# Kernel tuning notes

Hardware: AMD Instinct MI355X
Metric: run time of the kernel (lower is better)

The kernel has to match this reference:

```python
import jax, jax.numpy as jnp
import numpy as np

DIM = 64
NUM_HEAD = 4
C_IN = 2 * DIM                      # dim * proj_ratio
N_PER_HEAD = C_IN // NUM_HEAD       # 32
M_TRI = N_PER_HEAD * (N_PER_HEAD + 1) // 2   # 528
C_POOL = NUM_HEAD * M_TRI           # 2112 == dim*(dim+2)/2
EPS = 1e-5


def setup_inputs() -> dict:
    key = jax.random.key(0)
    ks = jax.random.split(key, 8)
    B, H, W = 4, 128, 128
    x = jax.random.normal(ks[0], (B, C_IN, H, W), dtype=jnp.float32)
    norm1_w = 1.0 + 0.1 * jax.random.normal(ks[1], (C_IN,), dtype=jnp.float32)
    norm1_b = 0.1 * jax.random.normal(ks[2], (C_IN,), dtype=jnp.float32)
    dr_w = 0.02 * jax.random.normal(ks[3], (DIM, C_POOL), dtype=jnp.float32)
    dr_b = 0.02 * jax.random.normal(ks[4], (DIM,), dtype=jnp.float32)
    norm2_w = 1.0 + 0.1 * jax.random.normal(ks[5], (DIM,), dtype=jnp.float32)
    norm2_b = 0.1 * jax.random.normal(ks[6], (DIM,), dtype=jnp.float32)
    fc1_w = 0.05 * jax.random.normal(ks[7], (DIM, DIM), dtype=jnp.float32)
    fc1_b = jnp.zeros((DIM,), dtype=jnp.float32)
    return {"x": x, "norm1_w": norm1_w, "norm1_b": norm1_b,
            "dr_w": dr_w, "dr_b": dr_b,
            "norm2_w": norm2_w, "norm2_b": norm2_b,
            "fc1_w": fc1_w, "fc1_b": fc1_b}


def _layernorm_nchw(x, g, b):
    # LayerNorm over channel dim of NCHW tensor (torch permutes to NHWC first)
    xt = jnp.transpose(x, (0, 2, 3, 1))
    mu = jnp.mean(xt, axis=-1, keepdims=True)
    var = jnp.mean(jnp.square(xt - mu), axis=-1, keepdims=True)
    y = (xt - mu) / jnp.sqrt(var + EPS) * g + b
    return jnp.transpose(y, (0, 3, 1, 2))


def reference(x, norm1_w, norm1_b, dr_w, dr_b, norm2_w, norm2_b, fc1_w, fc1_b):
    B, C, H, W = x.shape
    L = H * W
    nh, n = NUM_HEAD, N_PER_HEAD

    # --- norm1 ---
    x = _layernorm_nchw(x, norm1_w, norm1_b)

    # --- MHSP ---
    # channel shuffle: group = C // num_head = n, group_C = num_head
    x = x.reshape(B, n, nh, H, W).transpose(0, 2, 1, 3, 4).reshape(B, C, H, W)
    # unfold with kernel=1, stride=1, pad=0 is a pure reshape -> [B, L, C]
    t = x.reshape(B, C, L).transpose(0, 2, 1).reshape(B, L, nh, n)
    # per-position per-head rank-1 outer product: [B, L, nh, n, n]
    outer = jnp.einsum('blhi,blhj->blhij', t, t)
    # sparse_mapping matmul == gather of upper-triangle entries (row-major i<=j)
    iu, ju = np.triu_indices(n)
    pf = outer[..., iu, ju]                      # [B, L, nh, m]
    pf = pf.reshape(B, L, nh * M_TRI).transpose(0, 2, 1).reshape(B, C_POOL, H, W)

    # --- CTM token mixer ---
    C2 = C_POOL
    y = pf.reshape(B, nh, C2 // nh, L)
    yn = y / jnp.linalg.norm(y, axis=2, keepdims=True)
    mid = L // 2
    x0 = yn[..., mid]                            # [B, nh, C2/nh]
    attn = jnp.einsum('bhc,bhcl->bhl', x0, yn)   # [B, nh, L]
    attn = jax.nn.softmax(attn, axis=-1)[:, :, None, :]
    y = (y * attn * float(L)).reshape(B, C2, H, W)

    # --- dimension reduction (1x1 conv) ---
    z = jnp.einsum('bchw,oc->bohw', y, dr_w) + dr_b[None, :, None, None]

    # --- norm2 + LightMlp (1x1 conv + GELU) ---
    z = _layernorm_nchw(z, norm2_w, norm2_b)
    z = jnp.einsum('bchw,oc->bohw', z, fc1_w) + fc1_b[None, :, None, None]
    z = jax.nn.gelu(z, approximate=False)
    return z
```

## Files before the change

### kernel.cpp

```cpp
#include <hip/hip_runtime.h>
#include <hip/hip_bf16.h>
#include <math.h>

#define B_    4
#define CIN   128
#define L_    16384
#define NH    4
#define NN    32
#define MT    528
#define CP    2112
#define DIM_  64
#define LT    64
#define MID   8192
#define EPS_  1e-5f

#define KPH   640
#define KTOT  2560
#define WSWN  (KTOT * DIM_)
#define FSWN  (2 * 4 * 64 * 8)
#define LOGITS_BLOCKS 1024
#define PREP_BLOCKS   656

typedef __attribute__((ext_vector_type(8))) short short8;
typedef __attribute__((ext_vector_type(4))) float float4v;
typedef __attribute__((ext_vector_type(4))) unsigned uint4v;

__device__ inline unsigned short f2bf(float f) {
  unsigned u = __float_as_uint(f);
  unsigned r = (u + 0x7fffu + ((u >> 16) & 1u)) >> 16;
  return (unsigned short)r;
}

__device__ inline float bflo(unsigned u) { float f; asm("v_lshlrev_b32 %0, 16, %1" : "=v"(f) : "v"(u)); return f; }
__device__ inline float bfhi(unsigned u) { float f; asm("v_and_b32 %0, 0xffff0000, %1" : "=v"(f) : "v"(u)); return f; }

__device__ inline void kb_decode(int id, int& i, int& jb) {
  if (id < 32)      { i = id >> 2;               jb = id & 3; }
  else if (id < 56) { int r = id - 32; int d = r / 3; i = 8 + d;  jb = 1 + (r - 3 * d); }
  else if (id < 72) { int r = id - 56; i = 16 + (r >> 1); jb = 2 + (r & 1); }
  else              { i = 24 + (id - 72);         jb = 3; }
}

__global__ __launch_bounds__(256) void k_pre(const float* __restrict__ dr_w,
                                             const float* __restrict__ fc1_w,
                                             const float* __restrict__ x,
                                             const float* __restrict__ g1,
                                             const float* __restrict__ b1,
                                             unsigned short* __restrict__ wsw,
                                             unsigned short* __restrict__ fsw,
                                             float* __restrict__ ws_a,
                                             float* __restrict__ ws_bsum) {
  if (blockIdx.x >= LOGITS_BLOCKS) {
    int s = (blockIdx.x - LOGITS_BLOCKS) * 256 + threadIdx.x;
    if (s < WSWN) {
      int j    = s & 7;
      int lane = (s >> 3) & 63;
      int ot   = (s >> 9) & 3;
      int ksg  = s >> 11;
      int o  = ot * 16 + (lane & 15);
      int h  = lane >> 4;
      int i, jb; kb_decode(ksg, i, jb);
      int jch = jb * 8 + j;
      float val = 0.f;
      if (jch >= i) {
        int fi = 32 * i - (i * (i - 1)) / 2;
        int m  = h * MT + fi + (jch - i);
        val = dr_w[(size_t)o * CP + m];
      }
      wsw[s] = f2bf(val);
    } else {
      int s2 = s - WSWN;
      int j    = s2 & 7;
      int lane = (s2 >> 3) & 63;
      int ot   = (s2 >> 9) & 3;
      int ks2  = s2 >> 11;
      int o = ot * 16 + (lane & 15);
      int c = ks2 * 32 + (lane >> 4) * 8 + j;
      fsw[s2] = f2bf(fc1_w[o * DIM_ + c]);
    }
    return;
  }
  int blk = blockIdx.x;
  int b = blk >> 8;
  int l0 = (blk & 255) << 6;
  int t = threadIdx.x;
  int l = t & 63, q = t >> 6;
  __shared__ float xs[CIN], smid[CIN];
  __shared__ float part[4][64], part2[4][64], mu_s[64], isd_s[64];
  __shared__ float musd[2];

  if (t < CIN) xs[t] = x[(size_t)b * CIN * L_ + (size_t)t * L_ + MID];

  float tv[32];
  const float* xb = x + (size_t)b * CIN * L_ + l0 + l;
  float s = 0.f, s2 = 0.f;
#pragma unroll
  for (int cc = 0; cc < 32; cc++) {
    float v = xb[(size_t)(cc * 4 + q) * L_];
    tv[cc] = v; s += v; s2 += v * v;
  }
  part[q][l] = s; part2[q][l] = s2;
  __syncthreads();
  if (t < 64) {
    float a = xs[t], bb = xs[t + 64];
    float ms = a + bb, ms2 = a * a + bb * bb;
#pragma unroll
    for (int mk = 1; mk < 64; mk <<= 1) {
      ms += __shfl_xor(ms, mk, 64);
      ms2 += __shfl_xor(ms2, mk, 64);
    }
    if (t == 0) {
      float mu = ms * (1.f / CIN);
      musd[0] = mu;
      musd[1] = rsqrtf(ms2 * (1.f / CIN) - mu * mu + EPS_);
    }
    float su = part[0][t] + part[1][t] + part[2][t] + part[3][t];
    float su2 = part2[0][t] + part2[1][t] + part2[2][t] + part2[3][t];
    float mu = su * (1.f / CIN);
    float var = su2 * (1.f / CIN) - mu * mu;
    mu_s[t] = mu; isd_s[t] = rsqrtf(var + EPS_);
  }
  __syncthreads();
  if (t < CIN) {
    int c = ((t & 31) << 2) + (t >> 5);
    smid[t] = (xs[c] - musd[0]) * musd[1] * g1[c] + b1[c];
  }
  {
    float mu = mu_s[l], isd = isd_s[l];
#pragma unroll
    for (int cc = 0; cc < 32; cc++) {
      int co = cc * 4 + q;
      tv[cc] = (tv[cc] - mu) * isd * g1[co] + b1[co];
    }
  }
  __syncthreads();
  float T2 = 0.f, T4 = 0.f, st = 0.f, sc2 = 0.f, S2 = 0.f, S4 = 0.f;
#pragma unroll
  for (int i = 0; i < 32; i++) {
    float si = smid[q * 32 + i];
    float ti = tv[i];
    float t2 = ti * ti;
    T2 += t2; T4 = fmaf(t2, t2, T4);
    float ci = si * ti;
    st += ci; sc2 = fmaf(ci, ci, sc2);
    float s2i = si * si;
    S2 += s2i; S4 = fmaf(s2i, s2i, S4);
  }
  float num = 0.5f * (st * st + sc2);
  float logit = num * rsqrtf(0.25f * (T2 * T2 + T4) * (S2 * S2 + S4));
  float e = expf(logit - 1.f);
  ws_a[((size_t)b * NH + q) * L_ + l0 + l] = e;
  float ws = e;
#pragma unroll
  for (int mk = 1; mk < 64; mk <<= 1) ws += __shfl_xor(ws, mk, 64);
  if (l == 0) ws_bsum[((size_t)b * NH + q) * 256 + (blk & 255)] = ws;
}

struct __align__(16) SmemM {
  union __align__(16) { unsigned short p2[4 * 5 * 4 * 16 * 8]; float zb[64 * 65]; } u1;
  unsigned short zn2[4 * 2 * 4 * 16 * 8];
  float part[4][64], part2[4][64], mu_s[64], isd_s[64];
};

__global__ __launch_bounds__(256) void k_main(const float* __restrict__ x,
      const float* __restrict__ g1, const float* __restrict__ b1,
      const float* __restrict__ dr_b,
      const float* __restrict__ g2, const float* __restrict__ b2,
      const float* __restrict__ fc1_b,
      const unsigned short* __restrict__ wsw, const unsigned short* __restrict__ fsw,
      const float* __restrict__ ws_a, const float* __restrict__ ws_bsum,
      float* __restrict__ out) {
  __shared__ SmemM sm;
  int blk = blockIdx.x;
  int b = blk >> 8;
  int l0 = (blk & 255) << 6;
  int t = threadIdx.x;
  int l = t & 63, q = t >> 6;

  float asum;
  {
    const float* bs = ws_bsum + ((size_t)b * NH + q) * 256;
    float a0 = bs[l] + bs[l + 64] + bs[l + 128] + bs[l + 192];
#pragma unroll
    for (int mk = 1; mk < 64; mk <<= 1) a0 += __shfl_xor(a0, mk, 64);
    asum = a0;
  }
  float e = ws_a[((size_t)b * NH + q) * L_ + l0 + l];
  float sa = sqrtf(e * ((float)L_ / asum));

  const float* xb = x + (size_t)b * CIN * L_ + l0 + l;
  unsigned tn16[16];
  float s = 0.f, s2 = 0.f;
#pragma unroll
  for (int r = 0; r < 16; r++) {
    float v0 = xb[(size_t)((2 * r) * 4 + q) * L_];
    float v1 = xb[(size_t)((2 * r + 1) * 4 + q) * L_];
    s += v0 + v1; s2 += v0 * v0 + v1 * v1;
    asm("v_cvt_pk_bf16_f32 %0, %1, %2" : "=v"(tn16[r]) : "v"(v0), "v"(v1));
  }
  sm.part[q][l] = s; sm.part2[q][l] = s2;
  __syncthreads();
  if (t < 64) {
    float su = sm.part[0][t] + sm.part[1][t] + sm.part[2][t] + sm.part[3][t];
    float su2 = sm.part2[0][t] + sm.part2[1][t] + sm.part2[2][t] + sm.part2[3][t];
    float mu = su * (1.f / CIN);
    float var = su2 * (1.f / CIN) - mu * mu;
    sm.mu_s[t] = mu; sm.isd_s[t] = rsqrtf(var + EPS_);
  }
  __syncthreads();
  {
    float mu = sm.mu_s[l], isd = sm.isd_s[l];
#pragma unroll
    for (int r = 0; r < 16; r++) {
      int c0 = (2 * r) * 4 + q, c1 = c0 + 4;
      float v0 = (bflo(tn16[r]) - mu) * isd * g1[c0] + b1[c0];
      float v1 = (bfhi(tn16[r]) - mu) * isd * g1[c1] + b1[c1];
      v0 *= sa; v1 *= sa;
      asm("v_cvt_pk_bf16_f32 %0, %1, %2" : "=v"(tn16[r]) : "v"(v0), "v"(v1));
    }
  }

  const int otp = q & 1, ltp = q >> 1;
  const int lta = ltp * 2, ltb = ltp * 2 + 1;
  float4v acc[2][2];
  acc[0][0] = (float4v)0.f; acc[0][1] = (float4v)0.f;
  acc[1][0] = (float4v)0.f; acc[1][1] = (float4v)0.f;
  int tl = l;
  int ltile = l >> 4, n = l & 15;

#pragma unroll
  for (int p = 0; p < 16; p++) {
#pragma unroll
    for (int ks = 0; ks < 5; ks++) {
      const int g = p * 5 + ks;
      int i, jb; kb_decode(g, i, jb);
      unsigned uw = tn16[i >> 1];
      float ui = (i & 1) ? bfhi(uw) : bflo(uw);
      unsigned w0 = tn16[jb * 4 + 0], w1 = tn16[jb * 4 + 1];
      unsigned w2 = tn16[jb * 4 + 2], w3 = tn16[jb * 4 + 3];
      float f0 = bflo(w0) * ui, f1 = bfhi(w0) * ui;
      float f2 = bflo(w1) * ui, f3 = bfhi(w1) * ui;
      float f4 = bflo(w2) * ui, f5 = bfhi(w2) * ui;
      float f6 = bflo(w3) * ui, f7 = bfhi(w3) * ui;
      unsigned u0, u1, u2, u3;
      asm("v_cvt_pk_bf16_f32 %0, %1, %2" : "=v"(u0) : "v"(f0), "v"(f1));
      asm("v_cvt_pk_bf16_f32 %0, %1, %2" : "=v"(u1) : "v"(f2), "v"(f3));
      asm("v_cvt_pk_bf16_f32 %0, %1, %2" : "=v"(u2) : "v"(f4), "v"(f5));
      asm("v_cvt_pk_bf16_f32 %0, %1, %2" : "=v"(u3) : "v"(f6), "v"(f7));
      uint4v pv = {u0, u1, u2, u3};
      *(uint4v*)&sm.u1.p2[(((ltile * 5 + ks) * 4 + q) * 16 + n) * 8] = pv;
    }
    __syncthreads();
#pragma unroll
    for (int ks = 0; ks < 5; ks++) {
      const unsigned short* wk = wsw + (size_t)(p * 5 + ks) * 2048 + otp * 1024 + tl * 8;
      short8 a0 = *(const short8*)(wk);
      short8 a1 = *(const short8*)(wk + 512);
      short8 b0 = *(short8*)&sm.u1.p2[((lta * 5 + ks) * 64 + tl) * 8];
      short8 b1v = *(short8*)&sm.u1.p2[((ltb * 5 + ks) * 64 + tl) * 8];
      acc[0][0] = __builtin_amdgcn_mfma_f32_16x16x32_bf16(a0, b0,  acc[0][0], 0, 0, 0);
      acc[0][1] = __builtin_amdgcn_mfma_f32_16x16x32_bf16(a0, b1v, acc[0][1], 0, 0, 0);
      acc[1][0] = __builtin_amdgcn_mfma_f32_16x16x32_bf16(a1, b0,  acc[1][0], 0, 0, 0);
      acc[1][1] = __builtin_amdgcn_mfma_f32_16x16x32_bf16(a1, b1v, acc[1][1], 0, 0, 0);
    }
    __syncthreads();
  }

  int quad = tl >> 4;
#pragma unroll
  for (int oi = 0; oi < 2; oi++) {
#pragma unroll
    for (int li = 0; li < 2; li++) {
      int ot = otp * 2 + oi, ltx = ltp * 2 + li;
#pragma unroll
      for (int r = 0; r < 4; r++) {
        int o = ot * 16 + quad * 4 + r;
        sm.u1.zb[(ltx * 16 + n) * 65 + o] = acc[oi][li][r] + dr_b[o];
      }
    }
  }
  __syncthreads();
  {
    float ss = 0.f, ss2 = 0.f;
#pragma unroll
    for (int k = 0; k < 16; k++) {
      float v = sm.u1.zb[l * 65 + q * 16 + k];
      ss += v; ss2 += v * v;
    }
    sm.part[q][l] = ss; sm.part2[q][l] = ss2;
  }
  __syncthreads();
  if (t < 64) {
    float su = sm.part[0][t] + sm.part[1][t] + sm.part[2][t] + sm.part[3][t];
    float su2 = sm.part2[0][t] + sm.part2[1][t] + sm.part2[2][t] + sm.part2[3][t];
    float mu = su * (1.f / DIM_);
    float var = su2 * (1.f / DIM_) - mu * mu;
    sm.mu_s[t] = mu; sm.isd_s[t] = rsqrtf(var + EPS_);
  }
  __syncthreads();
  {
    float mu2 = sm.mu_s[l], isd2 = sm.isd_s[l];
#pragma unroll
    for (int kk = 0; kk < 2; kk++) {
      int kb2 = q * 2 + kk;
      int c0 = kb2 * 8;
      unsigned short pk[8];
#pragma unroll
      for (int e8 = 0; e8 < 8; e8++) {
        int c = c0 + e8;
        float v = (sm.u1.zb[l * 65 + c] - mu2) * isd2 * g2[c] + b2[c];
        pk[e8] = f2bf(v);
      }
      int ks2 = kb2 >> 2, qd2 = kb2 & 3;
      *(short8*)&sm.zn2[(((ltile * 2 + ks2) * 4 + qd2) * 16 + n) * 8] = *(short8*)pk;
    }
  }
  __syncthreads();
  float4v acc2[4];
  acc2[0] = (float4v)0.f; acc2[1] = (float4v)0.f; acc2[2] = (float4v)0.f; acc2[3] = (float4v)0.f;
#pragma unroll
  for (int ks2 = 0; ks2 < 2; ks2++) {
    short8 bz = *(short8*)&sm.zn2[((q * 2 + ks2) * 64 + tl) * 8];
    const unsigned short* fk = fsw + ks2 * 2048 + tl * 8;
    short8 f0 = *(const short8*)(fk);
    short8 f1 = *(const short8*)(fk + 512);
    short8 f2 = *(const short8*)(fk + 1024);
    short8 f3 = *(const short8*)(fk + 1536);
    acc2[0] = __builtin_amdgcn_mfma_f32_16x16x32_bf16(f0, bz, acc2[0], 0, 0, 0);
    acc2[1] = __builtin_amdgcn_mfma_f32_16x16x32_bf16(f1, bz, acc2[1], 0, 0, 0);
    acc2[2] = __builtin_amdgcn_mfma_f32_16x16x32_bf16(f2, bz, acc2[2], 0, 0, 0);
    acc2[3] = __builtin_amdgcn_mfma_f32_16x16x32_bf16(f3, bz, acc2[3], 0, 0, 0);
  }
#pragma unroll
  for (int ot = 0; ot < 4; ot++) {
#pragma unroll
    for (int r = 0; r < 4; r++) {
      int o2 = ot * 16 + quad * 4 + r;
      float sv = acc2[ot][r] + fc1_b[o2];
      float g = 0.5f * sv * (1.f + erff(sv * 0.70710678118f));
      out[((size_t)b * DIM_ + o2) * L_ + l0 + q * 16 + n] = g;
    }
  }
}

extern "C" void kernel_launch(void* const* d_in, const int* in_sizes, int n_in,
                              void* d_out, int out_size, void* d_ws, size_t ws_size,
                              hipStream_t stream) {
  const float* x    = (const float*)d_in[0];
  const float* n1w  = (const float*)d_in[1];
  const float* n1b  = (const float*)d_in[2];
  const float* drw  = (const float*)d_in[3];
  const float* drb  = (const float*)d_in[4];
  const float* n2w  = (const float*)d_in[5];
  const float* n2b  = (const float*)d_in[6];
  const float* fc1w = (const float*)d_in[7];
  const float* fc1b = (const float*)d_in[8];
  float* out = (float*)d_out;
  float* ws = (float*)d_ws;
  float* ws_a    = ws;
  float* ws_bsum = ws_a + (size_t)B_ * NH * L_;
  unsigned short* wsw = (unsigned short*)(ws_bsum + B_ * NH * 256);
  unsigned short* fsw = wsw + WSWN;

  hipLaunchKernelGGL(k_pre, dim3(LOGITS_BLOCKS + PREP_BLOCKS), dim3(256), 0, stream,
                     drw, fc1w, x, n1w, n1b, wsw, fsw, ws_a, ws_bsum);
  hipLaunchKernelGGL(k_main, dim3(B_ * (L_ / LT)), dim3(256), 0, stream,
                     x, n1w, n1b, drb, n2w, n2b, fc1b, wsw, fsw, ws_a, ws_bsum, out);
}
```

Baseline: 132.1 us.

## Switch bf16 MFMA path to fp16 with packed half products and fewer syncs

Replaces bf16 storage and MFMA with fp16 throughout the main kernel and the pre-swizzled weights. The outer-product features are now built with packed half multiplies straight from fp16 registers, avoiding per-element float unpack, multiply and repack. The k-loop staging is regrouped from 16 phases of 5 k-steps to 8 phases of 10, which doubles the shared staging buffer and halves the number of barriers. The fp16 range could overflow or lose precision on large products or weights.

```diff
diff --git a/kernel.cpp b/kernel.cpp
--- a/kernel.cpp
+++ b/kernel.cpp
@@ -24,15 +24,17 @@
 typedef __attribute__((ext_vector_type(8))) short short8;
 typedef __attribute__((ext_vector_type(4))) float float4v;
 typedef __attribute__((ext_vector_type(4))) unsigned uint4v;
-
-__device__ inline unsigned short f2bf(float f) {
-  unsigned u = __float_as_uint(f);
-  unsigned r = (u + 0x7fffu + ((u >> 16) & 1u)) >> 16;
-  return (unsigned short)r;
-}
-
-__device__ inline float bflo(unsigned u) { float f; asm("v_lshlrev_b32 %0, 16, %1" : "=v"(f) : "v"(u)); return f; }
-__device__ inline float bfhi(unsigned u) { float f; asm("v_and_b32 %0, 0xffff0000, %1" : "=v"(f) : "v"(u)); return f; }
+typedef __attribute__((ext_vector_type(2))) _Float16 h2;
+typedef __attribute__((ext_vector_type(8))) _Float16 half8;
+
+__device__ inline unsigned short f2h(float f) {
+  _Float16 h = (_Float16)f;
+  return __builtin_bit_cast(unsigned short, h);
+}
+
+__device__ inline h2 pkrtz(float a, float b) {
+  return __builtin_bit_cast(h2, __builtin_amdgcn_cvt_pkrtz(a, b));
+}
 
 __device__ inline void kb_decode(int id, int& i, int& jb) {
   if (id < 32)      { i = id >> 2;               jb = id & 3; }
@@ -67,7 +69,7 @@
         int m  = h * MT + fi + (jch - i);
         val = dr_w[(size_t)o * CP + m];
       }
-      wsw[s] = f2bf(val);
+      wsw[s] = f2h(val);
     } else {
       int s2 = s - WSWN;
       int j    = s2 & 7;
@@ -76,7 +78,7 @@
       int ks2  = s2 >> 11;
       int o = ot * 16 + (lane & 15);
       int c = ks2 * 32 + (lane >> 4) * 8 + j;
-      fsw[s2] = f2bf(fc1_w[o * DIM_ + c]);
+      fsw[s2] = f2h(fc1_w[o * DIM_ + c]);
     }
     return;
   }
@@ -157,7 +159,7 @@
 }
 
 struct __align__(16) SmemM {
-  union __align__(16) { unsigned short p2[4 * 5 * 4 * 16 * 8]; float zb[64 * 65]; } u1;
+  union __align__(16) { unsigned short p2[4 * 10 * 4 * 16 * 8]; float zb[64 * 65]; } u1;
   unsigned short zn2[4 * 2 * 4 * 16 * 8];
   float part[4][64], part2[4][64], mu_s[64], isd_s[64];
 };
@@ -189,14 +191,14 @@
   float sa = sqrtf(e * ((float)L_ / asum));
 
   const float* xb = x + (size_t)b * CIN * L_ + l0 + l;
-  unsigned tn16[16];
+  h2 tnh[16];
   float s = 0.f, s2 = 0.f;
 #pragma unroll
   for (int r = 0; r < 16; r++) {
     float v0 = xb[(size_t)((2 * r) * 4 + q) * L_];
     float v1 = xb[(size_t)((2 * r + 1) * 4 + q) * L_];
     s += v0 + v1; s2 += v0 * v0 + v1 * v1;
-    asm("v_cvt_pk_bf16_f32 %0, %1, %2" : "=v"(tn16[r]) : "v"(v0), "v"(v1));
+    tnh[r] = pkrtz(v0, v1);
   }
   sm.part[q][l] = s; sm.part2[q][l] = s2;
   __syncthreads();
@@ -213,10 +215,10 @@
 #pragma unroll
     for (int r = 0; r < 16; r++) {
       int c0 = (2 * r) * 4 + q, c1 = c0 + 4;
-      float v0 = (bflo(tn16[r]) - mu) * isd * g1[c0] + b1[c0];
-      float v1 = (bfhi(tn16[r]) - mu) * isd * g1[c1] + b1[c1];
+      float v0 = ((float)tnh[r][0] - mu) * isd * g1[c0] + b1[c0];
+      float v1 = ((float)tnh[r][1] - mu) * isd * g1[c1] + b1[c1];
       v0 *= sa; v1 *= sa;
-      asm("v_cvt_pk_bf16_f32 %0, %1, %2" : "=v"(tn16[r]) : "v"(v0), "v"(v1));
+      tnh[r] = pkrtz(v0, v1);
     }
   }
 
@@ -229,39 +231,33 @@
   int ltile = l >> 4, n = l & 15;
 
 #pragma unroll
-  for (int p = 0; p < 16; p++) {
-#pragma unroll
-    for (int ks = 0; ks < 5; ks++) {
-      const int g = p * 5 + ks;
+  for (int p = 0; p < 8; p++) {
+#pragma unroll
+    for (int ks = 0; ks < 10; ks++) {
+      const int g = p * 10 + ks;
       int i, jb; kb_decode(g, i, jb);
-      unsigned uw = tn16[i >> 1];
-      float ui = (i & 1) ? bfhi(uw) : bflo(uw);
-      unsigned w0 = tn16[jb * 4 + 0], w1 = tn16[jb * 4 + 1];
-      unsigned w2 = tn16[jb * 4 + 2], w3 = tn16[jb * 4 + 3];
-      float f0 = bflo(w0) * ui, f1 = bfhi(w0) * ui;
-      float f2 = bflo(w1) * ui, f3 = bfhi(w1) * ui;
-      float f4 = bflo(w2) * ui, f5 = bfhi(w2) * ui;
-      float f6 = bflo(w3) * ui, f7 = bfhi(w3) * ui;
-      unsigned u0, u1, u2, u3;
-      asm("v_cvt_pk_bf16_f32 %0, %1, %2" : "=v"(u0) : "v"(f0), "v"(f1));
-      asm("v_cvt_pk_bf16_f32 %0, %1, %2" : "=v"(u1) : "v"(f2), "v"(f3));
-      asm("v_cvt_pk_bf16_f32 %0, %1, %2" : "=v"(u2) : "v"(f4), "v"(f5));
-      asm("v_cvt_pk_bf16_f32 %0, %1, %2" : "=v"(u3) : "v"(f6), "v"(f7));
-      uint4v pv = {u0, u1, u2, u3};
-      *(uint4v*)&sm.u1.p2[(((ltile * 5 + ks) * 4 + q) * 16 + n) * 8] = pv;
+      _Float16 uh = tnh[i >> 1][i & 1];
+      h2 uu = {uh, uh};
+      h2 p0 = uu * tnh[jb * 4 + 0];
+      h2 p1 = uu * tnh[jb * 4 + 1];
+      h2 p2v = uu * tnh[jb * 4 + 2];
+      h2 p3 = uu * tnh[jb * 4 + 3];
+      uint4v pv = {__builtin_bit_cast(unsigned, p0), __builtin_bit_cast(unsigned, p1),
+                   __builtin_bit_cast(unsigned, p2v), __builtin_bit_cast(unsigned, p3)};
+      *(uint4v*)&sm.u1.p2[(((ltile * 10 + ks) * 4 + q) * 16 + n) * 8] = pv;
     }
     __syncthreads();
 #pragma unroll
-    for (int ks = 0; ks < 5; ks++) {
-      const unsigned short* wk = wsw + (size_t)(p * 5 + ks) * 2048 + otp * 1024 + tl * 8;
-      short8 a0 = *(const short8*)(wk);
-      short8 a1 = *(const short8*)(wk + 512);
-      short8 b0 = *(short8*)&sm.u1.p2[((lta * 5 + ks) * 64 + tl) * 8];
-      short8 b1v = *(short8*)&sm.u1.p2[((ltb * 5 + ks) * 64 + tl) * 8];
-      acc[0][0] = __builtin_amdgcn_mfma_f32_16x16x32_bf16(a0, b0,  acc[0][0], 0, 0, 0);
-      acc[0][1] = __builtin_amdgcn_mfma_f32_16x16x32_bf16(a0, b1v, acc[0][1], 0, 0, 0);
-      acc[1][0] = __builtin_amdgcn_mfma_f32_16x16x32_bf16(a1, b0,  acc[1][0], 0, 0, 0);
-      acc[1][1] = __builtin_amdgcn_mfma_f32_16x16x32_bf16(a1, b1v, acc[1][1], 0, 0, 0);
+    for (int ks = 0; ks < 10; ks++) {
+      const unsigned short* wk = wsw + (size_t)(p * 10 + ks) * 2048 + otp * 1024 + tl * 8;
+      half8 a0 = *(const half8*)(wk);
+      half8 a1 = *(const half8*)(wk + 512);
+      half8 b0 = *(half8*)&sm.u1.p2[((lta * 10 + ks) * 64 + tl) * 8];
+      half8 b1v = *(half8*)&sm.u1.p2[((ltb * 10 + ks) * 64 + tl) * 8];
+      acc[0][0] = __builtin_amdgcn_mfma_f32_16x16x32_f16(a0, b0,  acc[0][0], 0, 0, 0);
+      acc[0][1] = __builtin_amdgcn_mfma_f32_16x16x32_f16(a0, b1v, acc[0][1], 0, 0, 0);
+      acc[1][0] = __builtin_amdgcn_mfma_f32_16x16x32_f16(a1, b0,  acc[1][0], 0, 0, 0);
+      acc[1][1] = __builtin_amdgcn_mfma_f32_16x16x32_f16(a1, b1v, acc[1][1], 0, 0, 0);
     }
     __syncthreads();
   }
@@ -309,7 +305,7 @@
       for (int e8 = 0; e8 < 8; e8++) {
         int c = c0 + e8;
         float v = (sm.u1.zb[l * 65 + c] - mu2) * isd2 * g2[c] + b2[c];
-        pk[e8] = f2bf(v);
+        pk[e8] = f2h(v);
       }
       int ks2 = kb2 >> 2, qd2 = kb2 & 3;
       *(short8*)&sm.zn2[(((ltile * 2 + ks2) * 4 + qd2) * 16 + n) * 8] = *(short8*)pk;
@@ -320,16 +316,16 @@
   acc2[0] = (float4v)0.f; acc2[1] = (float4v)0.f; acc2[2] = (float4v)0.f; acc2[3] = (float4v)0.f;
 #pragma unroll
   for (int ks2 = 0; ks2 < 2; ks2++) {
-    short8 bz = *(short8*)&sm.zn2[((q * 2 + ks2) * 64 + tl) * 8];
+    half8 bz = *(half8*)&sm.zn2[((q * 2 + ks2) * 64 + tl) * 8];
     const unsigned short* fk = fsw + ks2 * 2048 + tl * 8;
-    short8 f0 = *(const short8*)(fk);
-    short8 f1 = *(const short8*)(fk + 512);
-    short8 f2 = *(const short8*)(fk + 1024);
-    short8 f3 = *(const short8*)(fk + 1536);
-    acc2[0] = __builtin_amdgcn_mfma_f32_16x16x32_bf16(f0, bz, acc2[0], 0, 0, 0);
-    acc2[1] = __builtin_amdgcn_mfma_f32_16x16x32_bf16(f1, bz, acc2[1], 0, 0, 0);
-    acc2[2] = __builtin_amdgcn_mfma_f32_16x16x32_bf16(f2, bz, acc2[2], 0, 0, 0);
-    acc2[3] = __builtin_amdgcn_mfma_f32_16x16x32_bf16(f3, bz, acc2[3], 0, 0, 0);
+    half8 f0 = *(const half8*)(fk);
+    half8 f1 = *(const half8*)(fk + 512);
+    half8 f2 = *(const half8*)(fk + 1024);
+    half8 f3 = *(const half8*)(fk + 1536);
+    acc2[0] = __builtin_amdgcn_mfma_f32_16x16x32_f16(f0, bz, acc2[0], 0, 0, 0);
+    acc2[1] = __builtin_amdgcn_mfma_f32_16x16x32_f16(f1, bz, acc2[1], 0, 0, 0);
+    acc2[2] = __builtin_amdgcn_mfma_f32_16x16x32_f16(f2, bz, acc2[2], 0, 0, 0);
+    acc2[3] = __builtin_amdgcn_mfma_f32_16x16x32_f16(f3, bz, acc2[3], 0, 0, 0);
   }
 #pragma unroll
   for (int ot = 0; ot < 4; ot++) {
```

Measured after the change: 143.2 us. +8.5%, slower.
